# Kernel tuning notes

Hardware: AMD Instinct MI355X
Metric: run time of the kernel (lower is better)

Reference implementation:

```python
import jax, jax.numpy as jnp
import numpy as np

B, S, E, H = 1, 2048, 512, 8
D = E // H
N = B * S
WIN_HALF = 32  # attention_window 64 -> +/-32
ALPHA = 0.1
LN_EPS = 1e-12
NEG_INF = -1e9


def _build_window_edges():
    # windowed graph: dst i attends to src j with |i-j| <= WIN_HALF, within each batch block
    i = np.arange(S)
    offs = np.arange(-WIN_HALF, WIN_HALF + 1)
    src = i[:, None] + offs[None, :]
    dst = np.broadcast_to(i[:, None], src.shape)
    valid = (src >= 0) & (src < S)
    src, dst = src[valid], dst[valid]
    srcs, dsts = [], []
    for b in range(B):
        srcs.append(src + b * S)
        dsts.append(dst + b * S)
    return (np.concatenate(srcs).astype(np.int32),
            np.concatenate(dsts).astype(np.int32))


def setup_inputs() -> dict:
    key = jax.random.key(0)
    ks = jax.random.split(key, 12)
    sc = 1.0 / np.sqrt(E)
    src_np, dst_np = _build_window_edges()
    return {
        "hidden_states": jax.random.normal(ks[0], (B, S, E), dtype=jnp.float32),
        "attention_mask": jnp.zeros((B, S), dtype=jnp.float32),
        "edge_src": jnp.asarray(src_np),
        "edge_dst": jnp.asarray(dst_np),
        "Wq": jax.random.normal(ks[1], (E, E), dtype=jnp.float32) * sc,
        "bq": jnp.zeros((E,), dtype=jnp.float32),
        "Wk": jax.random.normal(ks[2], (E, E), dtype=jnp.float32) * sc,
        "bk": jnp.zeros((E,), dtype=jnp.float32),
        "Wv": jax.random.normal(ks[3], (E, E), dtype=jnp.float32) * sc,
        "bv": jnp.zeros((E,), dtype=jnp.float32),
        "Wo": jax.random.normal(ks[4], (E, E), dtype=jnp.float32) * sc,
        "bo": jnp.zeros((E,), dtype=jnp.float32),
        "ln_g": jnp.ones((E,), dtype=jnp.float32),
        "ln_b": jnp.zeros((E,), dtype=jnp.float32),
    }


def reference(hidden_states, attention_mask, edge_src, edge_dst,
              Wq, bq, Wk, bk, Wv, bv, Wo, bo, ln_g, ln_b):
    x = hidden_states  # (B,S,E); node ordering n = b*S + s (matches torch reshape)
    q = ((x @ Wq + bq) / jnp.sqrt(jnp.asarray(D, x.dtype))).reshape(N, H, D)
    k = (x @ Wk + bk).reshape(N, H, D)
    v = (x @ Wv + bv).reshape(N, H, D)

    mask = (attention_mask >= 0).reshape(N)  # bool per node

    # u_dot_v('k','q','score'): per-edge, per-head dot product
    score = jnp.einsum('ehd,ehd->eh', k[edge_src], q[edge_dst])  # (Eg,H)
    score = jnp.where(mask[edge_src][:, None], score, NEG_INF)

    # edge_softmax over incoming edges of each destination node
    smax = jax.ops.segment_max(score, edge_dst, num_segments=N)
    p = jnp.exp(score - smax[edge_dst])
    denom = jax.ops.segment_sum(p, edge_dst, num_segments=N)
    p = p / denom[edge_dst]  # (Eg,H)

    # 5 diffusion steps: h <- A h, blended with residual v (dropout off in eval)
    h = v
    for _ in range(5):
        m = h[edge_src] * p[:, :, None]                      # u_mul_e
        h = jax.ops.segment_sum(m, edge_dst, num_segments=N)  # sum('m','h')
        h = (1.0 - ALPHA) * h + ALPHA * v

    attn = h.reshape(B, S, E)

    # DiffuserSelfOutput: dense -> residual add -> LayerNorm
    y = attn @ Wo + bo + hidden_states
    mu = y.mean(-1, keepdims=True)
    var = ((y - mu) ** 2).mean(-1, keepdims=True)
    out = (y - mu) * jax.lax.rsqrt(var + LN_EPS) * ln_g + ln_b
    return out
```

## Files before the change

### kernel.cpp

```cpp
#include <hip/hip_runtime.h>
#include <math.h>

#define S_LEN 2048
#define E_DIM 512
#define NE (S_LEN * E_DIM)
#define H_NUM 8
#define WH 32
#define NOFF 65
#define PROW (H_NUM * NOFF)
#define PN (S_LEN * PROW)

typedef float f32x4 __attribute__((ext_vector_type(4)));
typedef short short8 __attribute__((ext_vector_type(8)));

__device__ __forceinline__ unsigned short f2bf(float f) {
    union { float f; unsigned u; } cv; cv.f = f;
    unsigned u = cv.u;
    u += 0x7fffu + ((u >> 16) & 1u);
    return (unsigned short)(u >> 16);
}
__device__ __forceinline__ unsigned pk2(float x, float y) {
    return (unsigned)f2bf(x) | ((unsigned)f2bf(y) << 16);
}

__device__ __forceinline__ void mfma_gemm_f32(
    const float* __restrict__ A, const float* __restrict__ W,
    const float* __restrict__ bias, float* __restrict__ C,
    float scale, int m0, int n0)
{
    __shared__ unsigned short As[64 * 40];
    __shared__ unsigned short Bs[64 * 40];
    const int tid = threadIdx.x;
    const int lane = tid & 63, wave = tid >> 6;
    const int quad = lane >> 4, l16 = lane & 15;
    const int wr = (wave >> 1) * 32, wc = (wave & 1) * 32;
    const int ar = tid >> 2, ac = (tid & 3) * 8;
    const int bn = tid & 63, bk0 = (tid >> 6) * 8;

    f32x4 acc00 = {0.f,0.f,0.f,0.f}, acc01 = acc00, acc10 = acc00, acc11 = acc00;

    for (int kk = 0; kk < E_DIM; kk += 32) {
        float4 a0 = *(const float4*)(A + (size_t)(m0 + ar) * E_DIM + kk + ac);
        float4 a1 = *(const float4*)(A + (size_t)(m0 + ar) * E_DIM + kk + ac + 4);
        float b[8];
#pragma unroll
        for (int j = 0; j < 8; ++j)
            b[j] = W[(size_t)(kk + bk0 + j) * E_DIM + n0 + bn];
        __syncthreads();
        uint4 ap; ap.x = pk2(a0.x, a0.y); ap.y = pk2(a0.z, a0.w);
        ap.z = pk2(a1.x, a1.y); ap.w = pk2(a1.z, a1.w);
        *(uint4*)(As + ar * 40 + ac) = ap;
        uint4 bp; bp.x = pk2(b[0], b[1]); bp.y = pk2(b[2], b[3]);
        bp.z = pk2(b[4], b[5]); bp.w = pk2(b[6], b[7]);
        *(uint4*)(Bs + bn * 40 + bk0) = bp;
        __syncthreads();
        short8 fa0 = *(const short8*)(As + (wr + l16) * 40 + quad * 8);
        short8 fa1 = *(const short8*)(As + (wr + 16 + l16) * 40 + quad * 8);
        short8 fb0 = *(const short8*)(Bs + (wc + l16) * 40 + quad * 8);
        short8 fb1 = *(const short8*)(Bs + (wc + 16 + l16) * 40 + quad * 8);
        acc00 = __builtin_amdgcn_mfma_f32_16x16x32_bf16(fa0, fb0, acc00, 0, 0, 0);
        acc01 = __builtin_amdgcn_mfma_f32_16x16x32_bf16(fa0, fb1, acc01, 0, 0, 0);
        acc10 = __builtin_amdgcn_mfma_f32_16x16x32_bf16(fa1, fb0, acc10, 0, 0, 0);
        acc11 = __builtin_amdgcn_mfma_f32_16x16x32_bf16(fa1, fb1, acc11, 0, 0, 0);
    }

#pragma unroll
    for (int mi = 0; mi < 2; ++mi) {
#pragma unroll
        for (int ni = 0; ni < 2; ++ni) {
            f32x4 a = (mi == 0) ? ((ni == 0) ? acc00 : acc01)
                                : ((ni == 0) ? acc10 : acc11);
            int n = n0 + wc + ni * 16 + l16;
            float bval = bias[n];
#pragma unroll
            for (int r = 0; r < 4; ++r) {
                int m = m0 + wr + mi * 16 + quad * 4 + r;
                C[(size_t)m * E_DIM + n] = (a[r] + bval) * scale;
            }
        }
    }
}

__global__ __launch_bounds__(256)
void qkv_gemm(const float* __restrict__ x,
              const float* __restrict__ Wq, const float* __restrict__ bq,
              const float* __restrict__ Wk, const float* __restrict__ bk,
              const float* __restrict__ Wv, const float* __restrict__ bv,
              float* __restrict__ q, float* __restrict__ k, float* __restrict__ v)
{
    const float* W; const float* b; float* o; float sc;
    if (blockIdx.z == 0)      { W = Wq; b = bq; o = q; sc = 0.125f; }
    else if (blockIdx.z == 1) { W = Wk; b = bk; o = k; sc = 1.0f; }
    else                      { W = Wv; b = bv; o = v; sc = 1.0f; }
    mfma_gemm_f32(x, W, b, o, sc, blockIdx.y * 64, blockIdx.x * 64);
}

#define SDN 32
__global__ __launch_bounds__(256)
void scores_d1(const float* __restrict__ q, const float* __restrict__ k,
               const float* __restrict__ v, const float* __restrict__ amask,
               float* __restrict__ P, float* __restrict__ hA)
{
    const int i0 = blockIdx.x * SDN;
    const int h  = blockIdx.y;
    const int tid = threadIdx.x;
    __shared__ float ks[96 * 68];
    __shared__ float am[96];
    __shared__ float sc[SDN * 66];
    __shared__ float smx[SDN], sidn[SDN];
    __shared__ float ps[SDN * NOFF];

    for (int e = tid; e < 96 * 16; e += 256) {
        int lr = e >> 4, c4 = e & 15;
        int j = i0 - WH + lr;
        int jc = min(max(j, 0), S_LEN - 1);
        *(float4*)(ks + lr * 68 + c4 * 4) =
            *(const float4*)(k + (size_t)jc * E_DIM + h * 64 + c4 * 4);
    }
    if (tid < 96) {
        int j = i0 - WH + tid;
        am[tid] = (j >= 0 && j < S_LEN) ? amask[j] : -1.0f;
    }

    const int dst = tid >> 3;
    const int og  = tid & 7;
    float4 qreg[16];
    {
        const float4* qrow = (const float4*)(q + (size_t)(i0 + dst) * E_DIM + h * 64);
#pragma unroll
        for (int t = 0; t < 16; ++t) qreg[t] = qrow[t];
    }
    __syncthreads();

    for (int off = og; off < NOFF; off += 8) {
        int j = i0 + dst + off - WH;
        float s;
        if (j < 0 || j >= S_LEN) {
            s = -INFINITY;
        } else {
            int lr = dst + off;
            const float4* kr = (const float4*)(ks + lr * 68);
            float acc = 0.f;
#pragma unroll
            for (int t = 0; t < 16; ++t) {
                float4 a = qreg[t], bb = kr[t];
                acc += a.x * bb.x + a.y * bb.y + a.z * bb.z + a.w * bb.w;
            }
            s = (am[lr] >= 0.f) ? acc : -1e9f;
        }
        sc[dst * 66 + off] = s;
    }
    __syncthreads();

    for (int e = tid; e < 96 * 16; e += 256) {
        int lr = e >> 4, c4 = e & 15;
        int j = i0 - WH + lr;
        int jc = min(max(j, 0), S_LEN - 1);
        *(float4*)(ks + lr * 68 + c4 * 4) =
            *(const float4*)(v + (size_t)jc * E_DIM + h * 64 + c4 * 4);
    }
    if (tid < SDN) {
        float mx = -INFINITY;
        for (int o = 0; o < NOFF; ++o) mx = fmaxf(mx, sc[tid * 66 + o]);
        float dn = 0.f;
        for (int o = 0; o < NOFF; ++o) dn += expf(sc[tid * 66 + o] - mx);
        smx[tid] = mx; sidn[tid] = 1.f / dn;
    }
    __syncthreads();

    for (int e = tid; e < SDN * NOFF; e += 256) {
        int d = e / NOFF, off = e - d * NOFF;
        float pv = expf(sc[d * 66 + off] - smx[d]) * sidn[d];
        P[(size_t)(i0 + d) * PROW + h * NOFF + off] = pv;
        ps[e] = pv;
    }
    __syncthreads();

    {
        const int ci = tid & 15;
        const int ob = (tid >> 4) * 2;
        float4 a0 = {0,0,0,0}, a1 = a0;
        for (int lr = ob; lr < ob + 66; ++lr) {
            float4 hval = *(const float4*)(ks + lr * 68 + ci * 4);
            int o0 = lr - ob;
            if (o0 <= 64) {
                float p = ps[ob * NOFF + o0];
                a0.x += p * hval.x; a0.y += p * hval.y; a0.z += p * hval.z; a0.w += p * hval.w;
            }
            int o1 = o0 - 1;
            if ((unsigned)o1 <= 64u) {
                float p = ps[(ob + 1) * NOFF + o1];
                a1.x += p * hval.x; a1.y += p * hval.y; a1.z += p * hval.z; a1.w += p * hval.w;
            }
        }
#pragma unroll
        for (int r = 0; r < 2; ++r) {
            float4 a = r ? a1 : a0;
            float4 vv = *(const float4*)(ks + (WH + ob + r) * 68 + ci * 4);
            float4 o;
            o.x = 0.9f * a.x + 0.1f * vv.x;
            o.y = 0.9f * a.y + 0.1f * vv.y;
            o.z = 0.9f * a.z + 0.1f * vv.z;
            o.w = 0.9f * a.w + 0.1f * vv.w;
            *(float4*)(hA + (size_t)(i0 + ob + r) * E_DIM + h * 64 + ci * 4) = o;
        }
    }
}

__global__ __launch_bounds__(512)
void diffuse3m(const float* __restrict__ hin, const float* __restrict__ v,
               const float* __restrict__ P, float* __restrict__ hout)
{
    __shared__ unsigned short inT[64 * 264];
    __shared__ unsigned short m1T[64 * 200];
    __shared__ unsigned short ps[192 * 66];
    unsigned short* m2T = inT;
    const int i0 = blockIdx.x * 64;
    const int h  = blockIdx.y;
    const int c0 = h * 64;
    const int tid  = threadIdx.x;
    const int lane = tid & 63, wave = tid >> 6;
    const int quad = lane >> 4, l16 = lane & 15;

    for (int e = tid; e < 128 * 16; e += 512) {
        int rp = (e >> 4) * 2, c4 = (e & 15) * 4;
        int ja = min(max(i0 - 96 + rp,     0), S_LEN - 1);
        int jb = min(max(i0 - 96 + rp + 1, 0), S_LEN - 1);
        float4 ha = *(const float4*)(hin + (size_t)ja * E_DIM + c0 + c4);
        float4 hb = *(const float4*)(hin + (size_t)jb * E_DIM + c0 + c4);
        *(unsigned*)(inT + (c4 + 0) * 264 + rp) = pk2(ha.x, hb.x);
        *(unsigned*)(inT + (c4 + 1) * 264 + rp) = pk2(ha.y, hb.y);
        *(unsigned*)(inT + (c4 + 2) * 264 + rp) = pk2(ha.z, hb.z);
        *(unsigned*)(inT + (c4 + 3) * 264 + rp) = pk2(ha.w, hb.w);
    }
    for (int e = tid; e < 192 * 33; e += 512) {
        int mr = e / 33, t = e - mr * 33;
        int jc = min(max(i0 - 64 + mr, 0), S_LEN - 1);
        const float* pr = P + (size_t)jc * PROW + h * NOFF;
        if (t < 32)
            *(unsigned*)(ps + mr * 66 + t * 2) = pk2(pr[t * 2], pr[t * 2 + 1]);
        else
            ps[mr * 66 + 64] = f2bf(pr[64]);
    }
    __syncthreads();

#pragma unroll
    for (int uu = 0; uu < 3; ++uu) {
        int u = wave + uu * 8;
        int mtb = (u >> 1) * 16;
        int ntb = (u & 1) * 32;
        f32x4 a0 = {0.f,0.f,0.f,0.f}, a1 = a0;
        int ks0 = mtb >> 5;
        const int m = mtb + l16;
#pragma unroll
        for (int t = 0; t < 3; ++t) {
            int k0q = (ks0 + t) * 32 + quad * 8;
            short8 fa;
#pragma unroll
            for (int j = 0; j < 8; ++j) {
                int idx = k0q + j - m;
                int idc = min(max(idx, 0), 64);
                unsigned short pv = ps[m * 66 + idc];
                fa[j] = ((unsigned)idx <= 64u) ? (short)pv : (short)0;
            }
            short8 fb0 = *(const short8*)(inT + (ntb + l16) * 264 + k0q);
            short8 fb1 = *(const short8*)(inT + (ntb + 16 + l16) * 264 + k0q);
            a0 = __builtin_amdgcn_mfma_f32_16x16x32_bf16(fa, fb0, a0, 0, 0, 0);
            a1 = __builtin_amdgcn_mfma_f32_16x16x32_bf16(fa, fb1, a1, 0, 0, 0);
        }
#pragma unroll
        for (int nt = 0; nt < 2; ++nt) {
            f32x4 a = nt ? a1 : a0;
            int n = ntb + nt * 16 + l16;
            float o[4];
#pragma unroll
            for (int r = 0; r < 4; ++r) {
                int gm = min(max(i0 - 64 + mtb + quad * 4 + r, 0), S_LEN - 1);
                o[r] = 0.9f * a[r] + 0.1f * v[(size_t)gm * E_DIM + c0 + n];
            }
            *(unsigned*)(m1T + n * 200 + mtb + quad * 4)     = pk2(o[0], o[1]);
            *(unsigned*)(m1T + n * 200 + mtb + quad * 4 + 2) = pk2(o[2], o[3]);
        }
    }
    __syncthreads();

#pragma unroll
    for (int uu = 0; uu < 2; ++uu) {
        int u = wave + uu * 8;
        int mtb = (u >> 1) * 16;
        int ntb = (u & 1) * 32;
        f32x4 a0 = {0.f,0.f,0.f,0.f}, a1 = a0;
        int ks0 = mtb >> 5;
        const int m = mtb + l16;
#pragma unroll
        for (int t = 0; t < 3; ++t) {
            int k0q = (ks0 + t) * 32 + quad * 8;
            short8 fa;
#pragma unroll
            for (int j = 0; j < 8; ++j) {
                int idx = k0q + j - m;
                int idc = min(max(idx, 0), 64);
                unsigned short pv = ps[(m + 32) * 66 + idc];
                fa[j] = ((unsigned)idx <= 64u) ? (short)pv : (short)0;
            }
            short8 fb0 = *(const short8*)(m1T + (ntb + l16) * 200 + k0q);
            short8 fb1 = *(const short8*)(m1T + (ntb + 16 + l16) * 200 + k0q);
            a0 = __builtin_amdgcn_mfma_f32_16x16x32_bf16(fa, fb0, a0, 0, 0, 0);
            a1 = __builtin_amdgcn_mfma_f32_16x16x32_bf16(fa, fb1, a1, 0, 0, 0);
        }
        __syncthreads();
#pragma unroll
        for (int nt = 0; nt < 2; ++nt) {
            f32x4 a = nt ? a1 : a0;
            int n = ntb + nt * 16 + l16;
            float o[4];
#pragma unroll
            for (int r = 0; r < 4; ++r) {
                int gm = min(max(i0 - 32 + mtb + quad * 4 + r, 0), S_LEN - 1);
                o[r] = 0.9f * a[r] + 0.1f * v[(size_t)gm * E_DIM + c0 + n];
            }
            *(unsigned*)(m2T + n * 136 + mtb + quad * 4)     = pk2(o[0], o[1]);
            *(unsigned*)(m2T + n * 136 + mtb + quad * 4 + 2) = pk2(o[2], o[3]);
        }
    }
    __syncthreads();

    {
        int u = wave;
        int mtb = (u >> 1) * 16;
        int ntb = (u & 1) * 32;
        f32x4 a0 = {0.f,0.f,0.f,0.f}, a1 = a0;
        int ks0 = mtb >> 5;
        const int m = mtb + l16;
#pragma unroll
        for (int t = 0; t < 3; ++t) {
            int k0q = (ks0 + t) * 32 + quad * 8;
            short8 fa;
#pragma unroll
            for (int j = 0; j < 8; ++j) {
                int idx = k0q + j - m;
                int idc = min(max(idx, 0), 64);
                unsigned short pv = ps[(m + 64) * 66 + idc];
                fa[j] = ((unsigned)idx <= 64u) ? (short)pv : (short)0;
            }
            short8 fb0 = *(const short8*)(m2T + (ntb + l16) * 136 + k0q);
            short8 fb1 = *(const short8*)(m2T + (ntb + 16 + l16) * 136 + k0q);
            a0 = __builtin_amdgcn_mfma_f32_16x16x32_bf16(fa, fb0, a0, 0, 0, 0);
            a1 = __builtin_amdgcn_mfma_f32_16x16x32_bf16(fa, fb1, a1, 0, 0, 0);
        }
#pragma unroll
        for (int nt = 0; nt < 2; ++nt) {
            f32x4 a = nt ? a1 : a0;
            int n = ntb + nt * 16 + l16;
#pragma unroll
            for (int r = 0; r < 4; ++r) {
                int gm = i0 + mtb + quad * 4 + r;
                size_t base = (size_t)gm * E_DIM + c0 + n;
                hout[base] = 0.9f * a[r] + 0.1f * v[base];
            }
        }
    }
}

__global__ __launch_bounds__(512)
void oln3(const float* __restrict__ h4, const float* __restrict__ v,
          const float* __restrict__ P, const float* __restrict__ Wo,
          const float* __restrict__ bo, const float* __restrict__ x,
          const float* __restrict__ g, const float* __restrict__ lb,
          float* __restrict__ out)
{
    __shared__ unsigned short As[16 * 40];
    __shared__ unsigned short Bs[512 * 40];
    __shared__ unsigned short h4T[32 * 96];
    __shared__ unsigned short ps16[16 * 528];
    __shared__ float rsum[8][16], rsq[8][16];
    const int tid = threadIdx.x;
    const int lane = tid & 63, wave = tid >> 6;
    const int quad = lane >> 4, l16 = lane & 15;
    const int m0 = blockIdx.x * 16;
    const int n = tid;

    {
        int col = tid >> 4, r = tid & 15;
        h4T[col * 96 + 80 + r] = 0;
    }
    for (int e = tid; e < 16 * 260; e += 512) {
        int mr = e / 260, t = e - mr * 260;
        const float* pr = P + (size_t)(m0 + mr) * PROW;
        *(unsigned*)(ps16 + mr * 528 + t * 2) = pk2(pr[t * 2], pr[t * 2 + 1]);
    }

    f32x4 acc[4];
#pragma unroll
    for (int t = 0; t < 4; ++t) acc[t] = (f32x4){0.f,0.f,0.f,0.f};

    for (int kk = 0; kk < E_DIM; kk += 32) {
        const int hd = kk >> 6;
        float4 hv0, hv1;
        {
            int r = tid >> 3, c4 = (tid & 7) * 4;
            int jc = min(max(m0 - 32 + r, 0), S_LEN - 1);
            hv0 = *(const float4*)(h4 + (size_t)jc * E_DIM + kk + c4);
        }
        if (tid < 128) {
            int e = tid + 512;
            int r = e >> 3, c4 = (e & 7) * 4;
            int jc = min(max(m0 - 32 + r, 0), S_LEN - 1);
            hv1 = *(const float4*)(h4 + (size_t)jc * E_DIM + kk + c4);
        }
        float bcol[32];
#pragma unroll
        for (int j = 0; j < 32; ++j)
            bcol[j] = Wo[(size_t)(kk + j) * E_DIM + n];
        __syncthreads();
        {
            int r = tid >> 3, c4 = (tid & 7) * 4;
            h4T[(c4 + 0) * 96 + r] = f2bf(hv0.x);
            h4T[(c4 + 1) * 96 + r] = f2bf(hv0.y);
            h4T[(c4 + 2) * 96 + r] = f2bf(hv0.z);
            h4T[(c4 + 3) * 96 + r] = f2bf(hv0.w);
        }
        if (tid < 128) {
            int e = tid + 512;
            int r = e >> 3, c4 = (e & 7) * 4;
            h4T[(c4 + 0) * 96 + r] = f2bf(hv1.x);
            h4T[(c4 + 1) * 96 + r] = f2bf(hv1.y);
            h4T[(c4 + 2) * 96 + r] = f2bf(hv1.z);
            h4T[(c4 + 3) * 96 + r] = f2bf(hv1.w);
        }
#pragma unroll
        for (int t = 0; t < 4; ++t) {
            uint4 bp;
            bp.x = pk2(bcol[t*8+0], bcol[t*8+1]); bp.y = pk2(bcol[t*8+2], bcol[t*8+3]);
            bp.z = pk2(bcol[t*8+4], bcol[t*8+5]); bp.w = pk2(bcol[t*8+6], bcol[t*8+7]);
            *(uint4*)(Bs + n * 40 + t * 8) = bp;
        }
        __syncthreads();

        if (wave < 2) {
            const int ntb = wave * 16;
            f32x4 ba = {0.f,0.f,0.f,0.f};
#pragma unroll
            for (int t = 0; t < 3; ++t) {
                int k0q = t * 32 + quad * 8;
                short8 fa;
#pragma unroll
                for (int j = 0; j < 8; ++j) {
                    int idx = k0q + j - l16;
                    int idc = min(max(idx, 0), 64);
                    unsigned short pv = ps16[l16 * 528 + hd * NOFF + idc];
                    fa[j] = ((unsigned)idx <= 64u) ? (short)pv : (short)0;
                }
                short8 fb = *(const short8*)(h4T + (ntb + l16) * 96 + k0q);
                ba = __builtin_amdgcn_mfma_f32_16x16x32_bf16(fa, fb, ba, 0, 0, 0);
            }
#pragma unroll
            for (int r = 0; r < 4; ++r) {
                int m = quad * 4 + r;
                float vv = v[(size_t)(m0 + m) * E_DIM + kk + ntb + l16];
                As[m * 40 + ntb + l16] = f2bf(0.9f * ba[r] + 0.1f * vv);
            }
        }
        __syncthreads();

        short8 fa = *(const short8*)(As + l16 * 40 + quad * 8);
#pragma unroll
        for (int nt = 0; nt < 4; ++nt) {
            short8 fb = *(const short8*)(Bs + (wave * 64 + nt * 16 + l16) * 40 + quad * 8);
            acc[nt] = __builtin_amdgcn_mfma_f32_16x16x32_bf16(fa, fb, acc[nt], 0, 0, 0);
        }
    }

    float s[4] = {0.f,0.f,0.f,0.f}, s2[4] = {0.f,0.f,0.f,0.f};
#pragma unroll
    for (int nt = 0; nt < 4; ++nt) {
        int nc = wave * 64 + nt * 16 + l16;
        float bv = bo[nc];
#pragma unroll
        for (int r = 0; r < 4; ++r) {
            int m = m0 + quad * 4 + r;
            float vl = acc[nt][r] + bv + x[(size_t)m * E_DIM + nc];
            acc[nt][r] = vl;
            s[r] += vl; s2[r] += vl * vl;
        }
    }
#pragma unroll
    for (int o = 1; o < 16; o <<= 1) {
#pragma unroll
        for (int r = 0; r < 4; ++r) {
            s[r]  += __shfl_xor(s[r], o, 64);
            s2[r] += __shfl_xor(s2[r], o, 64);
        }
    }
    if (l16 == 0) {
#pragma unroll
        for (int r = 0; r < 4; ++r) {
            rsum[wave][quad * 4 + r] = s[r];
            rsq[wave][quad * 4 + r]  = s2[r];
        }
    }
    __syncthreads();
    float mu[4], rs[4];
#pragma unroll
    for (int r = 0; r < 4; ++r) {
        int rl = quad * 4 + r;
        float tot = 0.f, tot2 = 0.f;
#pragma unroll
        for (int w = 0; w < 8; ++w) { tot += rsum[w][rl]; tot2 += rsq[w][rl]; }
        float m_ = tot * (1.f / 512.f);
        float var = tot2 * (1.f / 512.f) - m_ * m_;
        mu[r] = m_; rs[r] = rsqrtf(var + 1e-12f);
    }
#pragma unroll
    for (int nt = 0; nt < 4; ++nt) {
        int nc = wave * 64 + nt * 16 + l16;
        float gv = g[nc], bbv = lb[nc];
#pragma unroll
        for (int r = 0; r < 4; ++r) {
            int m = m0 + quad * 4 + r;
            out[(size_t)m * E_DIM + nc] = (acc[nt][r] - mu[r]) * rs[r] * gv + bbv;
        }
    }
}

extern "C" void kernel_launch(void* const* d_in, const int* in_sizes, int n_in,
                              void* d_out, int out_size, void* d_ws, size_t ws_size,
                              hipStream_t stream)
{
    const float* x     = (const float*)d_in[0];
    const float* amask = (const float*)d_in[1];
    const float* Wq = (const float*)d_in[4];
    const float* bq = (const float*)d_in[5];
    const float* Wk = (const float*)d_in[6];
    const float* bk = (const float*)d_in[7];
    const float* Wv = (const float*)d_in[8];
    const float* bv = (const float*)d_in[9];
    const float* Wo = (const float*)d_in[10];
    const float* bo = (const float*)d_in[11];
    const float* lng = (const float*)d_in[12];
    const float* lnb = (const float*)d_in[13];
    float* out = (float*)d_out;

    float* ws = (float*)d_ws;
    float* q  = ws;
    float* k  = ws + (size_t)NE;
    float* v  = ws + (size_t)2 * NE;
    float* P  = ws + (size_t)3 * NE;
    float* hA = ws + (size_t)3 * NE + PN;
    float* hB = hA + (size_t)NE;

    qkv_gemm<<<dim3(8, 32, 3), 256, 0, stream>>>(x, Wq, bq, Wk, bk, Wv, bv, q, k, v);

    scores_d1<<<dim3(64, 8), 256, 0, stream>>>(q, k, v, amask, P, hA);

    diffuse3m<<<dim3(32, 8), 512, 0, stream>>>(hA, v, P, hB);

    oln3<<<128, 512, 0, stream>>>(hB, v, P, Wo, bo, x, lng, lnb, out);
}
```

Measured before the change: 170.9 us.

## Split final diffusion step from Wo GEMM and double-buffer Wo tiles

The fused last-diffusion-step plus output-projection kernel is restructured. The whole 16x512 diffused row block is first computed into shared memory in two half-width passes, with all 8 waves doing band MFMAs instead of 2. Wo is then streamed through a double-buffered shared tile, prefetching the next k-slice into registers while the current MFMAs run. This removes the idle waves and the per-k-step serialized load/convert stalls, at the cost of more shared memory (aliased buffers) and register pressure.

```diff
diff --git a/kernel.cpp b/kernel.cpp
--- a/kernel.cpp
+++ b/kernel.cpp
@@ -363,111 +363,130 @@
 }
 
 __global__ __launch_bounds__(512)
-void oln3(const float* __restrict__ h4, const float* __restrict__ v,
+void oln4(const float* __restrict__ h4, const float* __restrict__ v,
           const float* __restrict__ P, const float* __restrict__ Wo,
           const float* __restrict__ bo, const float* __restrict__ x,
           const float* __restrict__ g, const float* __restrict__ lb,
           float* __restrict__ out)
 {
-    __shared__ unsigned short As[16 * 40];
-    __shared__ unsigned short Bs[512 * 40];
-    __shared__ unsigned short h4T[32 * 96];
-    __shared__ unsigned short ps16[16 * 528];
+    __shared__ unsigned short As16[16 * 520];
+    __shared__ unsigned short Bs2[2][512 * 40];
     __shared__ float rsum[8][16], rsq[8][16];
+    unsigned short* h4T  = &Bs2[0][0];
+    unsigned short* ps16 = &Bs2[0][0] + 26624;
+
     const int tid = threadIdx.x;
     const int lane = tid & 63, wave = tid >> 6;
     const int quad = lane >> 4, l16 = lane & 15;
     const int m0 = blockIdx.x * 16;
     const int n = tid;
 
-    {
-        int col = tid >> 4, r = tid & 15;
-        h4T[col * 96 + 80 + r] = 0;
-    }
     for (int e = tid; e < 16 * 260; e += 512) {
         int mr = e / 260, t = e - mr * 260;
         const float* pr = P + (size_t)(m0 + mr) * PROW;
         *(unsigned*)(ps16 + mr * 528 + t * 2) = pk2(pr[t * 2], pr[t * 2 + 1]);
     }
 
-    f32x4 acc[4];
-#pragma unroll
-    for (int t = 0; t < 4; ++t) acc[t] = (f32x4){0.f,0.f,0.f,0.f};
-
-    for (int kk = 0; kk < E_DIM; kk += 32) {
-        const int hd = kk >> 6;
-        float4 hv0, hv1;
+    for (int hc = 0; hc < 2; ++hc) {
+        for (int e = tid; e < 64 * 64; e += 512) {
+            int r = e & 63, c4 = (e >> 6) * 4;
+            int row = min(max(m0 - 32 + r, 0), S_LEN - 1);
+            float4 hv = *(const float4*)(h4 + (size_t)row * E_DIM + hc * 256 + c4);
+            h4T[(c4 + 0) * 104 + r] = f2bf(hv.x);
+            h4T[(c4 + 1) * 104 + r] = f2bf(hv.y);
+            h4T[(c4 + 2) * 104 + r] = f2bf(hv.z);
+            h4T[(c4 + 3) * 104 + r] = f2bf(hv.w);
+        }
+        for (int e = tid; e < 32 * 64; e += 512) {
+            int r = 64 + (e & 31), c4 = (e >> 5) * 4;
+            int row = min(max(m0 - 32 + r, 0), S_LEN - 1);
+            float4 hv = *(const float4*)(h4 + (size_t)row * E_DIM + hc * 256 + c4);
+            h4T[(c4 + 0) * 104 + r] = f2bf(hv.x);
+            h4T[(c4 + 1) * 104 + r] = f2bf(hv.y);
+            h4T[(c4 + 2) * 104 + r] = f2bf(hv.z);
+            h4T[(c4 + 3) * 104 + r] = f2bf(hv.w);
+        }
+        __syncthreads();
+
         {
-            int r = tid >> 3, c4 = (tid & 7) * 4;
-            int jc = min(max(m0 - 32 + r, 0), S_LEN - 1);
-            hv0 = *(const float4*)(h4 + (size_t)jc * E_DIM + kk + c4);
-        }
-        if (tid < 128) {
-            int e = tid + 512;
-            int r = e >> 3, c4 = (e & 7) * 4;
-            int jc = min(max(m0 - 32 + r, 0), S_LEN - 1);
-            hv1 = *(const float4*)(h4 + (size_t)jc * E_DIM + kk + c4);
-        }
-        float bcol[32];
-#pragma unroll
-        for (int j = 0; j < 32; ++j)
-            bcol[j] = Wo[(size_t)(kk + j) * E_DIM + n];
-        __syncthreads();
-        {
-            int r = tid >> 3, c4 = (tid & 7) * 4;
-            h4T[(c4 + 0) * 96 + r] = f2bf(hv0.x);
-            h4T[(c4 + 1) * 96 + r] = f2bf(hv0.y);
-            h4T[(c4 + 2) * 96 + r] = f2bf(hv0.z);
-            h4T[(c4 + 3) * 96 + r] = f2bf(hv0.w);
-        }
-        if (tid < 128) {
-            int e = tid + 512;
-            int r = e >> 3, c4 = (e & 7) * 4;
-            h4T[(c4 + 0) * 96 + r] = f2bf(hv1.x);
-            h4T[(c4 + 1) * 96 + r] = f2bf(hv1.y);
-            h4T[(c4 + 2) * 96 + r] = f2bf(hv1.z);
-            h4T[(c4 + 3) * 96 + r] = f2bf(hv1.w);
-        }
-#pragma unroll
-        for (int t = 0; t < 4; ++t) {
-            uint4 bp;
-            bp.x = pk2(bcol[t*8+0], bcol[t*8+1]); bp.y = pk2(bcol[t*8+2], bcol[t*8+3]);
-            bp.z = pk2(bcol[t*8+4], bcol[t*8+5]); bp.w = pk2(bcol[t*8+6], bcol[t*8+7]);
-            *(uint4*)(Bs + n * 40 + t * 8) = bp;
-        }
-        __syncthreads();
-
-        if (wave < 2) {
-            const int ntb = wave * 16;
-            f32x4 ba = {0.f,0.f,0.f,0.f};
+            const int hd = hc * 4 + (wave >> 1);
+            short8 fa[3];
 #pragma unroll
             for (int t = 0; t < 3; ++t) {
                 int k0q = t * 32 + quad * 8;
-                short8 fa;
 #pragma unroll
                 for (int j = 0; j < 8; ++j) {
                     int idx = k0q + j - l16;
                     int idc = min(max(idx, 0), 64);
                     unsigned short pv = ps16[l16 * 528 + hd * NOFF + idc];
-                    fa[j] = ((unsigned)idx <= 64u) ? (short)pv : (short)0;
+                    fa[t][j] = ((unsigned)idx <= 64u) ? (short)pv : (short)0;
                 }
-                short8 fb = *(const short8*)(h4T + (ntb + l16) * 96 + k0q);
-                ba = __builtin_amdgcn_mfma_f32_16x16x32_bf16(fa, fb, ba, 0, 0, 0);
-            }
-#pragma unroll
-            for (int r = 0; r < 4; ++r) {
-                int m = quad * 4 + r;
-                float vv = v[(size_t)(m0 + m) * E_DIM + kk + ntb + l16];
-                As[m * 40 + ntb + l16] = f2bf(0.9f * ba[r] + 0.1f * vv);
+            }
+#pragma unroll
+            for (int nt = 0; nt < 2; ++nt) {
+                int lc = wave * 32 + nt * 16;
+                f32x4 ba = {0.f, 0.f, 0.f, 0.f};
+#pragma unroll
+                for (int t = 0; t < 3; ++t) {
+                    short8 fb = *(const short8*)(h4T + (lc + l16) * 104 + t * 32 + quad * 8);
+                    ba = __builtin_amdgcn_mfma_f32_16x16x32_bf16(fa[t], fb, ba, 0, 0, 0);
+                }
+                int gcol = hc * 256 + lc + l16;
+#pragma unroll
+                for (int r = 0; r < 4; ++r) {
+                    int m = quad * 4 + r;
+                    float vv = v[(size_t)(m0 + m) * E_DIM + gcol];
+                    As16[m * 520 + gcol] = f2bf(0.9f * ba[r] + 0.1f * vv);
+                }
             }
         }
         __syncthreads();
-
-        short8 fa = *(const short8*)(As + l16 * 40 + quad * 8);
+    }
+
+    {
+        float w0[32];
+#pragma unroll
+        for (int j = 0; j < 32; ++j)
+            w0[j] = Wo[(size_t)j * E_DIM + n];
+#pragma unroll
+        for (int t = 0; t < 4; ++t) {
+            uint4 bp;
+            bp.x = pk2(w0[t*8+0], w0[t*8+1]); bp.y = pk2(w0[t*8+2], w0[t*8+3]);
+            bp.z = pk2(w0[t*8+4], w0[t*8+5]); bp.w = pk2(w0[t*8+6], w0[t*8+7]);
+            *(uint4*)(&Bs2[0][0] + n * 40 + t * 8) = bp;
+        }
+    }
+
+    f32x4 acc[4];
+#pragma unroll
+    for (int t = 0; t < 4; ++t) acc[t] = (f32x4){0.f,0.f,0.f,0.f};
+
+#pragma unroll 2
+    for (int it = 0; it < 16; ++it) {
+        float wn[32];
+        if (it < 15) {
+#pragma unroll
+            for (int j = 0; j < 32; ++j)
+                wn[j] = Wo[(size_t)((it + 1) * 32 + j) * E_DIM + n];
+        }
+        __syncthreads();
+
+        short8 fa = *(const short8*)(As16 + l16 * 520 + it * 32 + quad * 8);
 #pragma unroll
         for (int nt = 0; nt < 4; ++nt) {
-            short8 fb = *(const short8*)(Bs + (wave * 64 + nt * 16 + l16) * 40 + quad * 8);
+            short8 fb = *(const short8*)(&Bs2[it & 1][0] +
+                                         (wave * 64 + nt * 16 + l16) * 40 + quad * 8);
             acc[nt] = __builtin_amdgcn_mfma_f32_16x16x32_bf16(fa, fb, acc[nt], 0, 0, 0);
+        }
+
+        if (it < 15) {
+#pragma unroll
+            for (int t = 0; t < 4; ++t) {
+                uint4 bp;
+                bp.x = pk2(wn[t*8+0], wn[t*8+1]); bp.y = pk2(wn[t*8+2], wn[t*8+3]);
+                bp.z = pk2(wn[t*8+4], wn[t*8+5]); bp.w = pk2(wn[t*8+6], wn[t*8+7]);
+                *(uint4*)(&Bs2[(it + 1) & 1][0] + n * 40 + t * 8) = bp;
+            }
         }
     }
 
@@ -555,5 +574,5 @@
 
     diffuse3m<<<dim3(32, 8), 512, 0, stream>>>(hA, v, P, hB);
 
-    oln3<<<128, 512, 0, stream>>>(hB, v, P, Wo, bo, x, lng, lnb, out);
-}
+    oln4<<<128, 512, 0, stream>>>(hB, v, P, Wo, bo, x, lng, lnb, out);
+}
```

New measurement: 170.7 us. About the same (-0.1%).
